# Performance work log

Measured on AMD Instinct MI355X. Metric: run time of the kernel, lower is better.

The kernel has to match this reference:

```python
import jax, jax.numpy as jnp
import numpy as np

N, E, H, C, F_IN, G = 20000, 320000, 8, 32, 41, 64
NEG_SLOPE = 0.2
BN_EPS = 1e-5


def setup_inputs() -> dict:
    key = jax.random.key(0)
    ks = jax.random.split(key, 32)
    s = 0.05
    d = {
        'x': jax.random.normal(ks[0], (N, F_IN), jnp.float32),
        'edge_index': jax.random.randint(ks[1], (2, E), 0, N, jnp.int32),
        'batch': jnp.sort(jax.random.randint(ks[2], (N,), 0, G, jnp.int32)),
        'graph_size': jax.random.uniform(ks[3], (G, 2), jnp.float32) * 10.0,
        'W1': jax.random.normal(ks[4], (F_IN, H * C), jnp.float32) * s,
        'a_src1': jax.random.normal(ks[5], (H, C), jnp.float32) * s,
        'a_dst1': jax.random.normal(ks[6], (H, C), jnp.float32) * s,
        'b1': jnp.zeros((H * C,), jnp.float32),
        'g1': jnp.ones((H * C,), jnp.float32),
        'be1': jnp.zeros((H * C,), jnp.float32),
        'W2': jax.random.normal(ks[7], (H * C, H * C), jnp.float32) * s,
        'a_src2': jax.random.normal(ks[8], (H, C), jnp.float32) * s,
        'a_dst2': jax.random.normal(ks[9], (H, C), jnp.float32) * s,
        'b2': jnp.zeros((H * C,), jnp.float32),
        'g2': jnp.ones((H * C,), jnp.float32),
        'be2': jnp.zeros((H * C,), jnp.float32),
        'fc1_w': jax.random.normal(ks[10], (2 * H * C + 2, 64), jnp.float32) * s,
        'fc1_b': jnp.zeros((64,), jnp.float32),
        'gf1': jnp.ones((64,), jnp.float32),
        'bf1': jnp.zeros((64,), jnp.float32),
        'fc2_w': jax.random.normal(ks[11], (64, 32), jnp.float32) * s,
        'fc2_b': jnp.zeros((32,), jnp.float32),
        'gf2': jnp.ones((32,), jnp.float32),
        'bf2': jnp.zeros((32,), jnp.float32),
        'fc3_w': jax.random.normal(ks[12], (32, 2), jnp.float32) * s,
        'fc3_b': jnp.zeros((2,), jnp.float32),
    }
    return d


def _bn_eval(x, gamma, beta):
    # eval-mode BatchNorm with running_mean=0, running_var=1
    inv = 1.0 / jnp.sqrt(1.0 + BN_EPS)
    return x * (gamma * inv) + beta


def _gat_layer(x, W, a_src, a_dst, bias, src, dst):
    h = (x @ W).reshape(N, H, C)                       # [N,H,C]
    s_src = jnp.einsum('nhc,hc->nh', h, a_src)         # [N,H]
    s_dst = jnp.einsum('nhc,hc->nh', h, a_dst)
    scores = jax.nn.leaky_relu(s_src[src] + s_dst[dst], NEG_SLOPE)  # [E+N,H]
    m = jax.ops.segment_max(scores, dst, num_segments=N)
    e = jnp.exp(scores - m[dst])
    denom = jax.ops.segment_sum(e, dst, num_segments=N)
    alpha = e / denom[dst]                             # [E+N,H]
    out = jax.ops.segment_sum(alpha[:, :, None] * h[src], dst, num_segments=N)
    return out.reshape(N, H * C) + bias


def reference(x, edge_index, batch, graph_size, W1, a_src1, a_dst1, b1, g1, be1,
              W2, a_src2, a_dst2, b2, g2, be2, fc1_w, fc1_b, gf1, bf1,
              fc2_w, fc2_b, gf2, bf2, fc3_w, fc3_b):
    # add self loops (PyG GATConv add_self_loops=True)
    loops = jnp.arange(N, dtype=edge_index.dtype)
    src = jnp.concatenate([edge_index[0], loops])
    dst = jnp.concatenate([edge_index[1], loops])

    h = _gat_layer(x, W1, a_src1, a_dst1, b1, src, dst)
    h = jax.nn.elu(_bn_eval(h, g1, be1))
    h = _gat_layer(h, W2, a_src2, a_dst2, b2, src, dst)
    h = jax.nn.elu(_bn_eval(h, g2, be2))

    # global mean + max pooling per graph
    counts = jax.ops.segment_sum(jnp.ones((N, 1), h.dtype), batch, num_segments=G)
    x_mean = jax.ops.segment_sum(h, batch, num_segments=G) / jnp.maximum(counts, 1.0)
    x_max = jax.ops.segment_max(h, batch, num_segments=G)
    p = jnp.concatenate([x_mean, x_max, graph_size], axis=1)  # [G, 514]

    z = jax.nn.relu(_bn_eval(p @ fc1_w + fc1_b, gf1, bf1))
    z = jax.nn.relu(_bn_eval(z @ fc2_w + fc2_b, gf2, bf2))
    logits = z @ fc3_w + fc3_b
    return logits
```

## Files before the change

kernel.cpp:

```cpp
#include <hip/hip_runtime.h>
#include <hip/hip_bf16.h>

#define N_NODES 20000
#define E_EDGES 320000
#define NH 8
#define NC 32
#define HC 256
#define FIN 41
#define NG 64
#define PCHUNK 16
#define NPAD 20032

typedef _Float16 f16x4 __attribute__((ext_vector_type(4)));
typedef _Float16 f16x8 __attribute__((ext_vector_type(8)));
typedef float f32x4v __attribute__((ext_vector_type(4)));


__global__ __launch_bounds__(512) void scanA(const int* __restrict__ cnt, int* partial) {
    __shared__ int red[512];
    int n = blockIdx.x * 512 + threadIdx.x;
    int v = (n < N_NODES) ? cnt[n] + 1 : 0;
    red[threadIdx.x] = v; __syncthreads();
    for (int off = 256; off > 0; off >>= 1) {
        if (threadIdx.x < off) red[threadIdx.x] += red[threadIdx.x + off];
        __syncthreads();
    }
    if (threadIdx.x == 0) partial[blockIdx.x] = red[0];
}

__global__ __launch_bounds__(512) void scanC(const int* __restrict__ cnt, const int* __restrict__ partial,
                                             int* row_ptr, int* cursor, int* colidx) {
    __shared__ int buf[512];
    __shared__ int pbase;
    int t = threadIdx.x;
    if (t < 64) {
        int v = (t < 40) ? partial[t] : 0;
        int own = v;
        for (int off = 1; off < 64; off <<= 1) {
            int y = __shfl_up(v, off);
            if (t >= off) v += y;
        }
        if (t == (int)blockIdx.x) pbase = v - own;
    }
    int n = blockIdx.x * 512 + t;
    int v = (n < N_NODES) ? cnt[n] + 1 : 0;
    int x = v;
    buf[t] = x; __syncthreads();
    for (int off = 1; off < 512; off <<= 1) {
        int y = (t >= off) ? buf[t - off] : 0;
        __syncthreads();
        x += y; buf[t] = x; __syncthreads();
    }
    int excl = pbase + x - v;
    if (n < N_NODES) {
        row_ptr[n] = excl;
        cursor[n] = excl + 1;
        colidx[excl] = n;
    }
    if (n == 0) row_ptr[N_NODES] = E_EDGES + N_NODES;
}

__global__ __launch_bounds__(256) void fill_csr(const int* __restrict__ ei, int* cursor, int* colidx) {
    int e = blockIdx.x * 256 + threadIdx.x;
    if (e >= E_EDGES) return;
    int d = ei[E_EDGES + e];
    int s = ei[e];
    int pos = atomicAdd(&cursor[d], 1);
    colidx[pos] = s;
}


__global__ __launch_bounds__(256) void prep(const float* __restrict__ W, _Float16* __restrict__ Wt,
                                            const float* __restrict__ fc1w, float* __restrict__ fc1wT,
                                            const int* __restrict__ batch, int* gstart, int* gend,
                                            const float* __restrict__ W1, _Float16* __restrict__ W1t,
                                            const float* __restrict__ x, _Float16* __restrict__ xpad,
                                            const int* __restrict__ ei, int* cnt) {
    __shared__ float tile[64][65];
    int b = blockIdx.x;
    int t = threadIdx.x;
    if (b < 16) {
        int tr = (b >> 2) * 64;
        int tc = (b & 3) * 64;
        int rr = t >> 6, cc = t & 63;
#pragma unroll
        for (int j = 0; j < 16; ++j) {
            int row = j * 4 + rr;
            tile[row][cc] = W[(size_t)(tr + row) * 256 + tc + cc];
        }
        __syncthreads();
#pragma unroll
        for (int j = 0; j < 16; ++j) {
            int row = j * 4 + rr;
            Wt[(size_t)(tc + row) * 256 + tr + cc] = (_Float16)tile[cc][row];
        }
    } else if (b < 145) {
        int id = (b - 16) * 256 + t;
        if (id < 64 * 514) {
            int u = id / 514, kk = id - u * 514;
            fc1wT[u * 520 + kk] = fc1w[kk * 64 + u];
        }
    } else if (b < 224) {
        int n = (b - 145) * 256 + t;
        if (n < N_NODES) {
            int bb = batch[n];
            if (n == 0) gstart[bb] = 0;
            else {
                int pb = batch[n - 1];
                if (pb != bb) { gstart[bb] = n; gend[pb] = n; }
            }
            if (n == N_NODES - 1) gend[bb] = N_NODES;
        }
    } else if (b < 288) {
        int id = (b - 224) * 256 + t;
        int n = id >> 6, k = id & 63;
        W1t[id] = (k < FIN) ? (_Float16)W1[k * 256 + n] : (_Float16)0.f;
    } else if (b < 914) {
        int row = (b - 288) * 32 + (t >> 3);
        int c8 = (t & 7) * 8;
        f16x8 v;
#pragma unroll
        for (int j = 0; j < 8; ++j) {
            int c = c8 + j;
            float f = (row < N_NODES && c < FIN) ? x[(size_t)row * FIN + c] : 0.f;
            v[j] = (_Float16)f;
        }
        if (row < NPAD) *(f16x8*)(xpad + (size_t)row * 64 + c8) = v;
    } else {
        int e = (b - 914) * 256 + t;
        if (e < E_EDGES) atomicAdd(&cnt[ei[E_EDGES + e]], 1);
    }
}


__global__ __launch_bounds__(256) void gemm256h(const _Float16* __restrict__ Xh,
                                                const _Float16* __restrict__ Wt,
                                                const float* __restrict__ a_src,
                                                const float* __restrict__ a_dst,
                                                _Float16* __restrict__ Hh,
                                                float* __restrict__ ssrc,
                                                float* __restrict__ sdst) {
    __shared__ _Float16 bs[128 * 272];
    int row0 = (blockIdx.x >> 1) * 64;
    int half = blockIdx.x & 1;
    int c0 = half * 128;
    int tid = threadIdx.x;
    int lane = tid & 63;
    int v = tid >> 6;
    int r16 = lane & 15;
    int kseg = lane >> 4;

#pragma unroll
    for (int i = 0; i < 16; ++i) {
        int chunk = i * 256 + tid;
        int c = chunk >> 5;
        int k = (chunk & 31) * 8;
        f16x8 xv = *(const f16x8*)(Wt + (size_t)(c0 + c) * 256 + k);
        *(f16x8*)(&bs[c * 272 + k]) = xv;
    }

    int arow = row0 + v * 16 + r16;
    const _Float16* XA = Xh + (size_t)arow * 256 + kseg * 8;
    f16x8 af[8];
#pragma unroll
    for (int s = 0; s < 8; ++s) af[s] = *(const f16x8*)(XA + s * 32);

    __syncthreads();

    f32x4v acc[8];
#pragma unroll
    for (int tn = 0; tn < 8; ++tn) acc[tn] = (f32x4v){0.f, 0.f, 0.f, 0.f};

#pragma unroll
    for (int tn = 0; tn < 8; ++tn) {
        f16x8 bf[8];
#pragma unroll
        for (int s = 0; s < 8; ++s)
            bf[s] = *(const f16x8*)(&bs[(tn * 16 + r16) * 272 + kseg * 8 + s * 32]);
#pragma unroll
        for (int s = 0; s < 8; ++s)
            acc[tn] = __builtin_amdgcn_mfma_f32_16x16x32_f16(af[s], bf[s], acc[tn], 0, 0, 0);
    }

#pragma unroll
    for (int hh = 0; hh < 4; ++hh) {
        float as0 = a_src[c0 + hh * 32 + r16], as1 = a_src[c0 + hh * 32 + 16 + r16];
        float ad0 = a_dst[c0 + hh * 32 + r16], ad1 = a_dst[c0 + hh * 32 + 16 + r16];
#pragma unroll
        for (int r = 0; r < 4; ++r) {
            float p = acc[2 * hh][r] * as0 + acc[2 * hh + 1][r] * as1;
            float q = acc[2 * hh][r] * ad0 + acc[2 * hh + 1][r] * ad1;
            p += __shfl_xor(p, 1); q += __shfl_xor(q, 1);
            p += __shfl_xor(p, 2); q += __shfl_xor(q, 2);
            p += __shfl_xor(p, 4); q += __shfl_xor(q, 4);
            p += __shfl_xor(p, 8); q += __shfl_xor(q, 8);
            int row = row0 + v * 16 + kseg * 4 + r;
            if (r16 == 0 && row < N_NODES) {
                ssrc[row * NH + half * 4 + hh] = p;
                sdst[row * NH + half * 4 + hh] = q;
            }
        }
    }

    __syncthreads();
    _Float16* hs = bs;
#pragma unroll
    for (int tn = 0; tn < 8; ++tn)
#pragma unroll
        for (int r = 0; r < 4; ++r)
            hs[(v * 16 + kseg * 4 + r) * 136 + tn * 16 + r16] = (_Float16)acc[tn][r];
    __syncthreads();
#pragma unroll
    for (int i = 0; i < 4; ++i) {
        int idx = i * 256 + tid;
        int row = idx >> 4;
        int c8 = (idx & 15) * 8;
        if (row0 + row < N_NODES) {
            f16x8 xv = *(const f16x8*)&hs[row * 136 + c8];
            *(f16x8*)(Hh + (size_t)(row0 + row) * 256 + c0 + c8) = xv;
        }
    }
}


__global__ __launch_bounds__(256) void gemm41h(const _Float16* __restrict__ Xh,
                                               const _Float16* __restrict__ W1t,
                                               const float* __restrict__ a_src,
                                               const float* __restrict__ a_dst,
                                               _Float16* __restrict__ Hh,
                                               float* __restrict__ ssrc,
                                               float* __restrict__ sdst) {
    __shared__ _Float16 bs[128 * 72];
    __shared__ _Float16 hs[64 * 136];
    int row0 = (blockIdx.x >> 1) * 64;
    int half = blockIdx.x & 1;
    int c0 = half * 128;
    int tid = threadIdx.x;
    int lane = tid & 63;
    int v = tid >> 6;
    int r16 = lane & 15;
    int kseg = lane >> 4;

#pragma unroll
    for (int i = 0; i < 4; ++i) {
        int chunk = i * 256 + tid;
        int c = chunk >> 3;
        int k = (chunk & 7) * 8;
        f16x8 xv = *(const f16x8*)(W1t + (size_t)(c0 + c) * 64 + k);
        *(f16x8*)(&bs[c * 72 + k]) = xv;
    }

    int arow = row0 + v * 16 + r16;
    const _Float16* XA = Xh + (size_t)arow * 64 + kseg * 8;
    f16x8 af[2];
    af[0] = *(const f16x8*)(XA);
    af[1] = *(const f16x8*)(XA + 32);

    __syncthreads();

    f32x4v acc[8];
#pragma unroll
    for (int tn = 0; tn < 8; ++tn) acc[tn] = (f32x4v){0.f, 0.f, 0.f, 0.f};

#pragma unroll
    for (int tn = 0; tn < 8; ++tn) {
        f16x8 bf0 = *(const f16x8*)(&bs[(tn * 16 + r16) * 72 + kseg * 8]);
        f16x8 bf1 = *(const f16x8*)(&bs[(tn * 16 + r16) * 72 + kseg * 8 + 32]);
        acc[tn] = __builtin_amdgcn_mfma_f32_16x16x32_f16(af[0], bf0, acc[tn], 0, 0, 0);
        acc[tn] = __builtin_amdgcn_mfma_f32_16x16x32_f16(af[1], bf1, acc[tn], 0, 0, 0);
    }

#pragma unroll
    for (int hh = 0; hh < 4; ++hh) {
        float as0 = a_src[c0 + hh * 32 + r16], as1 = a_src[c0 + hh * 32 + 16 + r16];
        float ad0 = a_dst[c0 + hh * 32 + r16], ad1 = a_dst[c0 + hh * 32 + 16 + r16];
#pragma unroll
        for (int r = 0; r < 4; ++r) {
            float p = acc[2 * hh][r] * as0 + acc[2 * hh + 1][r] * as1;
            float q = acc[2 * hh][r] * ad0 + acc[2 * hh + 1][r] * ad1;
            p += __shfl_xor(p, 1); q += __shfl_xor(q, 1);
            p += __shfl_xor(p, 2); q += __shfl_xor(q, 2);
            p += __shfl_xor(p, 4); q += __shfl_xor(q, 4);
            p += __shfl_xor(p, 8); q += __shfl_xor(q, 8);
            int row = row0 + v * 16 + kseg * 4 + r;
            if (r16 == 0 && row < N_NODES) {
                ssrc[row * NH + half * 4 + hh] = p;
                sdst[row * NH + half * 4 + hh] = q;
            }
        }
    }

    __syncthreads();
#pragma unroll
    for (int tn = 0; tn < 8; ++tn)
#pragma unroll
        for (int r = 0; r < 4; ++r)
            hs[(v * 16 + kseg * 4 + r) * 136 + tn * 16 + r16] = (_Float16)acc[tn][r];
    __syncthreads();
#pragma unroll
    for (int i = 0; i < 4; ++i) {
        int idx = i * 256 + tid;
        int row = idx >> 4;
        int c8 = (idx & 15) * 8;
        if (row0 + row < N_NODES) {
            f16x8 xv = *(const f16x8*)&hs[row * 136 + c8];
            *(f16x8*)(Hh + (size_t)(row0 + row) * 256 + c0 + c8) = xv;
        }
    }
}


__global__ __launch_bounds__(256) void gat_agg(const int* __restrict__ row_ptr,
                                               const int* __restrict__ colidx,
                                               const float* __restrict__ ssrc,
                                               const float* __restrict__ sdst,
                                               const _Float16* __restrict__ h,
                                               const float* __restrict__ bias,
                                               const float* __restrict__ gamma,
                                               const float* __restrict__ beta,
                                               _Float16* __restrict__ outh) {
    int wave = (blockIdx.x * blockDim.x + threadIdx.x) >> 6;
    int lane = threadIdx.x & 63;
    if (wave >= N_NODES) return;
    int n = wave;
    int beg = row_ptr[n], end = row_ptr[n + 1];
    int deg = end - beg;

    int hd = lane >> 3;
    float sd = sdst[n * NH + hd];
    int c = lane * 4;
    float acc0 = 0.f, acc1 = 0.f, acc2 = 0.f, acc3 = 0.f, denom = 0.f;

    int i = 0;
    for (; i + 8 <= deg; i += 8) {
        int sidx[8];
#pragma unroll
        for (int j = 0; j < 8; ++j) sidx[j] = colidx[beg + i + j];
        float wv[8];
#pragma unroll
        for (int j = 0; j < 8; ++j) {
            float v = ssrc[sidx[j] * NH + hd] + sd;
            v = (v >= 0.f) ? v : 0.2f * v;
            wv[j] = __expf(v);
        }
        f16x4 hv[8];
#pragma unroll
        for (int j = 0; j < 8; ++j) hv[j] = *reinterpret_cast<const f16x4*>(h + (size_t)sidx[j] * HC + c);
#pragma unroll
        for (int j = 0; j < 8; ++j) {
            denom += wv[j];
            acc0 += wv[j] * (float)hv[j][0];
            acc1 += wv[j] * (float)hv[j][1];
            acc2 += wv[j] * (float)hv[j][2];
            acc3 += wv[j] * (float)hv[j][3];
        }
    }
    for (; i < deg; ++i) {
        int s = colidx[beg + i];
        float v = ssrc[s * NH + hd] + sd;
        v = (v >= 0.f) ? v : 0.2f * v;
        float wgt = __expf(v);
        denom += wgt;
        const f16x4 hv = *reinterpret_cast<const f16x4*>(h + (size_t)s * HC + c);
        acc0 += wgt * (float)hv[0]; acc1 += wgt * (float)hv[1];
        acc2 += wgt * (float)hv[2]; acc3 += wgt * (float)hv[3];
    }
    float inv = 1.0f / denom;
    const float bninv = 0.99999500003749981f;
    float vals[4] = {acc0, acc1, acc2, acc3};
    f16x4 o;
#pragma unroll
    for (int j = 0; j < 4; ++j) {
        float v = vals[j] * inv + bias[c + j];
        v = v * (gamma[c + j] * bninv) + beta[c + j];
        v = (v > 0.f) ? v : (__expf(v) - 1.0f);
        o[j] = (_Float16)v;
    }
    *(f16x4*)(outh + (size_t)n * HC + c) = o;
}


__global__ __launch_bounds__(256) void pool_partial(const _Float16* __restrict__ h,
                                                    const int* __restrict__ gstart,
                                                    const int* __restrict__ gend,
                                                    float* __restrict__ psum,
                                                    float* __restrict__ pmax) {
    __shared__ float ssm[4][256];
    __shared__ float smx[4][256];
    int g = blockIdx.x >> 4;
    int c = blockIdx.x & (PCHUNK - 1);
    int t = threadIdx.x;
    int wv = t >> 6;
    int lane = t & 63;
    int c4 = lane * 4;
    int s = gstart[g], e = gend[g];
    int len = e - s;
    int n0 = s + (int)(((long long)len * c) / PCHUNK);
    int n1 = s + (int)(((long long)len * (c + 1)) / PCHUNK);
    float s0 = 0.f, s1 = 0.f, s2 = 0.f, s3 = 0.f;
    float m0 = -3.0e38f, m1 = -3.0e38f, m2 = -3.0e38f, m3 = -3.0e38f;
    for (int n = n0 + wv; n < n1; n += 4) {
        f16x4 v = *(const f16x4*)(h + (size_t)n * HC + c4);
        float f0 = (float)v[0], f1 = (float)v[1], f2 = (float)v[2], f3 = (float)v[3];
        s0 += f0; s1 += f1; s2 += f2; s3 += f3;
        m0 = fmaxf(m0, f0); m1 = fmaxf(m1, f1); m2 = fmaxf(m2, f2); m3 = fmaxf(m3, f3);
    }
    ssm[wv][c4] = s0; ssm[wv][c4 + 1] = s1; ssm[wv][c4 + 2] = s2; ssm[wv][c4 + 3] = s3;
    smx[wv][c4] = m0; smx[wv][c4 + 1] = m1; smx[wv][c4 + 2] = m2; smx[wv][c4 + 3] = m3;
    __syncthreads();
    float fs = ssm[0][t] + ssm[1][t] + ssm[2][t] + ssm[3][t];
    float fm = fmaxf(fmaxf(smx[0][t], smx[1][t]), fmaxf(smx[2][t], smx[3][t]));
    size_t base = (size_t)(g * PCHUNK + c) * HC + t;
    psum[base] = fs;
    pmax[base] = fm;
}


__global__ __launch_bounds__(256) void mlp(const float* __restrict__ psum,
                                           const float* __restrict__ pmax,
                                           const int* __restrict__ gstart,
                                           const int* __restrict__ gend,
                                           const float* __restrict__ gsz,
                                           const float* __restrict__ fc1wT, const float* __restrict__ fc1b,
                                           const float* __restrict__ gf1, const float* __restrict__ bf1,
                                           const float* __restrict__ fc2w, const float* __restrict__ fc2b,
                                           const float* __restrict__ gf2, const float* __restrict__ bf2,
                                           const float* __restrict__ fc3w, const float* __restrict__ fc3b,
                                           float* __restrict__ out) {
    __shared__ __align__(16) float pr[514];
    __shared__ float z1[64];
    __shared__ float zz2[8][32];
    __shared__ float z2[32];
    int g = blockIdx.x;
    int t = threadIdx.x;
    const float bninv = 0.99999500003749981f;

    {
        float s = 0.f, m = -3.0e38f;
#pragma unroll
        for (int c = 0; c < PCHUNK; ++c) {
            s += psum[(size_t)(g * PCHUNK + c) * HC + t];
            m = fmaxf(m, pmax[(size_t)(g * PCHUNK + c) * HC + t]);
        }
        float cnt = (float)(gend[g] - gstart[g]);
        pr[t] = s / fmaxf(cnt, 1.f);
        pr[256 + t] = m;
        if (t < 2) pr[512 + t] = gsz[g * 2 + t];
    }
    __syncthreads();

    {
        int wv = t >> 6, lane = t & 63;
        float4 pa = *reinterpret_cast<const float4*>(&pr[lane * 8]);
        float4 pb = *reinterpret_cast<const float4*>(&pr[lane * 8 + 4]);
#pragma unroll 4
        for (int i = 0; i < 16; ++i) {
            int u = wv * 16 + i;
            const float* wrow = fc1wT + u * 520;
            float4 wa = *reinterpret_cast<const float4*>(wrow + lane * 8);
            float4 wb = *reinterpret_cast<const float4*>(wrow + lane * 8 + 4);
            float a = pa.x * wa.x + pa.y * wa.y + pa.z * wa.z + pa.w * wa.w
                    + pb.x * wb.x + pb.y * wb.y + pb.z * wb.z + pb.w * wb.w;
            if (lane == 0) a += pr[512] * wrow[512] + pr[513] * wrow[513];
            a += __shfl_xor(a, 1); a += __shfl_xor(a, 2); a += __shfl_xor(a, 4);
            a += __shfl_xor(a, 8); a += __shfl_xor(a, 16); a += __shfl_xor(a, 32);
            if (lane == 0) {
                a += fc1b[u];
                a = a * (gf1[u] * bninv) + bf1[u];
                z1[u] = fmaxf(a, 0.f);
            }
        }
    }
    __syncthreads();

    {
        int u = t & 31, sp = t >> 5;
        float b = 0.f;
#pragma unroll
        for (int k = sp * 8; k < sp * 8 + 8; ++k) b += z1[k] * fc2w[k * 32 + u];
        zz2[sp][u] = b;
    }
    __syncthreads();
    if (t < 32) {
        float b = 0.f;
#pragma unroll
        for (int sp = 0; sp < 8; ++sp) b += zz2[sp][t];
        b += fc2b[t];
        b = b * (gf2[t] * bninv) + bf2[t];
        z2[t] = fmaxf(b, 0.f);
    }
    __syncthreads();

    if (t < 2) {
        float c = 0.f;
#pragma unroll
        for (int k = 0; k < 32; ++k) c += z2[k] * fc3w[k * 2 + t];
        out[g * 2 + t] = c + fc3b[t];
    }
}


extern "C" void kernel_launch(void* const* d_in, const int* in_sizes, int n_in,
                              void* d_out, int out_size, void* d_ws, size_t ws_size,
                              hipStream_t stream) {
    const float* x    = (const float*)d_in[0];
    const int*   ei   = (const int*)d_in[1];
    const int*   batch= (const int*)d_in[2];
    const float* gsz  = (const float*)d_in[3];
    const float* W1   = (const float*)d_in[4];
    const float* as1  = (const float*)d_in[5];
    const float* ad1  = (const float*)d_in[6];
    const float* b1   = (const float*)d_in[7];
    const float* g1   = (const float*)d_in[8];
    const float* be1  = (const float*)d_in[9];
    const float* W2   = (const float*)d_in[10];
    const float* as2  = (const float*)d_in[11];
    const float* ad2  = (const float*)d_in[12];
    const float* b2   = (const float*)d_in[13];
    const float* g2   = (const float*)d_in[14];
    const float* be2  = (const float*)d_in[15];
    const float* fc1w = (const float*)d_in[16];
    const float* fc1b = (const float*)d_in[17];
    const float* gf1  = (const float*)d_in[18];
    const float* bf1  = (const float*)d_in[19];
    const float* fc2w = (const float*)d_in[20];
    const float* fc2b = (const float*)d_in[21];
    const float* gf2  = (const float*)d_in[22];
    const float* bf2  = (const float*)d_in[23];
    const float* fc3w = (const float*)d_in[24];
    const float* fc3b = (const float*)d_in[25];
    float* out = (float*)d_out;

    char* w = (char*)d_ws;
    _Float16* h_half   = (_Float16*)w; w += (size_t)N_NODES * HC * 2;
    _Float16* act_half = (_Float16*)w; w += (size_t)N_NODES * HC * 2;
    _Float16* act2_half= (_Float16*)w; w += (size_t)N_NODES * HC * 2;
    _Float16* Wt       = (_Float16*)w; w += (size_t)HC * HC * 2;
    _Float16* W1t      = (_Float16*)w; w += (size_t)HC * 64 * 2;
    _Float16* xpad     = (_Float16*)w; w += (size_t)NPAD * 64 * 2;
    float* fc1wT       = (float*)w;    w += (size_t)64 * 520 * 4;
    float* ssrc        = (float*)w;    w += (size_t)N_NODES * NH * 4;
    float* sdst        = (float*)w;    w += (size_t)N_NODES * NH * 4;
    int* row_ptr  = (int*)w;   w += (size_t)(N_NODES + 1) * 4;
    int* cursor   = (int*)w;   w += (size_t)N_NODES * 4;
    int* cnt      = (int*)w;   w += (size_t)N_NODES * 4;
    int* gstart   = (int*)w;   w += 64 * 4;
    int* gend     = (int*)w;   w += 64 * 4;
    int* colidx   = (int*)w;   w += (size_t)(E_EDGES + N_NODES) * 4;
    int* partial  = (int*)w;   w += 64 * 4;

    float* psum = (float*)h_half;
    float* pmax = psum + (size_t)NG * PCHUNK * HC;

    hipMemsetAsync(cnt, 0, (size_t)(N_NODES + 128) * 4, stream);

    prep<<<2164, 256, 0, stream>>>(W2, Wt, fc1w, fc1wT, batch, gstart, gend, W1, W1t, x, xpad, ei, cnt);
    scanA<<<40, 512, 0, stream>>>(cnt, partial);
    scanC<<<40, 512, 0, stream>>>(cnt, partial, row_ptr, cursor, colidx);
    fill_csr<<<1250, 256, 0, stream>>>(ei, cursor, colidx);

    gemm41h<<<626, 256, 0, stream>>>(xpad, W1t, as1, ad1, h_half, ssrc, sdst);
    gat_agg<<<5000, 256, 0, stream>>>(row_ptr, colidx, ssrc, sdst, h_half, b1, g1, be1, act_half);

    gemm256h<<<626, 256, 0, stream>>>(act_half, Wt, as2, ad2, h_half, ssrc, sdst);
    gat_agg<<<5000, 256, 0, stream>>>(row_ptr, colidx, ssrc, sdst, h_half, b2, g2, be2, act2_half);

    pool_partial<<<NG * PCHUNK, 256, 0, stream>>>(act2_half, gstart, gend, psum, pmax);
    mlp<<<NG, 256, 0, stream>>>(psum, pmax, gstart, gend, gsz,
                                fc1wT, fc1b, gf1, bf1, fc2w, fc2b, gf2, bf2, fc3w, fc3b, out);
}
```

Before: 160.6 us.

## Fuse CSR fill into first GEMM launch and store attention scores in fp16

Merges the CSR fill kernel into the layer-1 GEMM launch as extra blocks, so the edge scatter runs alongside the GEMM and one launch is removed. Separately, the per-node source/destination attention scores are stored as fp16 instead of fp32, halving the bytes for the random gathers in the aggregation kernels. The fp16 scores lose some precision before leaky-relu and exp, which could shift softmax weights slightly.

```diff
diff --git a/kernel.cpp b/kernel.cpp
--- a/kernel.cpp
+++ b/kernel.cpp
@@ -58,15 +58,6 @@
         colidx[excl] = n;
     }
     if (n == 0) row_ptr[N_NODES] = E_EDGES + N_NODES;
-}
-
-__global__ __launch_bounds__(256) void fill_csr(const int* __restrict__ ei, int* cursor, int* colidx) {
-    int e = blockIdx.x * 256 + threadIdx.x;
-    if (e >= E_EDGES) return;
-    int d = ei[E_EDGES + e];
-    int s = ei[e];
-    int pos = atomicAdd(&cursor[d], 1);
-    colidx[pos] = s;
 }
 
 
@@ -138,8 +129,8 @@
                                                 const float* __restrict__ a_src,
                                                 const float* __restrict__ a_dst,
                                                 _Float16* __restrict__ Hh,
-                                                float* __restrict__ ssrc,
-                                                float* __restrict__ sdst) {
+                                                _Float16* __restrict__ ssrc,
+                                                _Float16* __restrict__ sdst) {
     __shared__ _Float16 bs[128 * 272];
     int row0 = (blockIdx.x >> 1) * 64;
     int half = blockIdx.x & 1;
@@ -196,8 +187,8 @@
             p += __shfl_xor(p, 8); q += __shfl_xor(q, 8);
             int row = row0 + v * 16 + kseg * 4 + r;
             if (r16 == 0 && row < N_NODES) {
-                ssrc[row * NH + half * 4 + hh] = p;
-                sdst[row * NH + half * 4 + hh] = q;
+                ssrc[row * NH + half * 4 + hh] = (_Float16)p;
+                sdst[row * NH + half * 4 + hh] = (_Float16)q;
             }
         }
     }
@@ -223,19 +214,34 @@
 }
 
 
-__global__ __launch_bounds__(256) void gemm41h(const _Float16* __restrict__ Xh,
-                                               const _Float16* __restrict__ W1t,
-                                               const float* __restrict__ a_src,
-                                               const float* __restrict__ a_dst,
-                                               _Float16* __restrict__ Hh,
-                                               float* __restrict__ ssrc,
-                                               float* __restrict__ sdst) {
+__global__ __launch_bounds__(256) void gemm41_fill(const _Float16* __restrict__ Xh,
+                                                   const _Float16* __restrict__ W1t,
+                                                   const float* __restrict__ a_src,
+                                                   const float* __restrict__ a_dst,
+                                                   _Float16* __restrict__ Hh,
+                                                   _Float16* __restrict__ ssrc,
+                                                   _Float16* __restrict__ sdst,
+                                                   const int* __restrict__ ei,
+                                                   int* cursor, int* colidx) {
     __shared__ _Float16 bs[128 * 72];
     __shared__ _Float16 hs[64 * 136];
-    int row0 = (blockIdx.x >> 1) * 64;
-    int half = blockIdx.x & 1;
+    int b = blockIdx.x;
+    int tid = threadIdx.x;
+
+    if (b >= 626) {
+        int e = (b - 626) * 256 + tid;
+        if (e < E_EDGES) {
+            int d = ei[E_EDGES + e];
+            int s = ei[e];
+            int pos = atomicAdd(&cursor[d], 1);
+            colidx[pos] = s;
+        }
+        return;
+    }
+
+    int row0 = (b >> 1) * 64;
+    int half = b & 1;
     int c0 = half * 128;
-    int tid = threadIdx.x;
     int lane = tid & 63;
     int v = tid >> 6;
     int r16 = lane & 15;
@@ -284,8 +290,8 @@
             p += __shfl_xor(p, 8); q += __shfl_xor(q, 8);
             int row = row0 + v * 16 + kseg * 4 + r;
             if (r16 == 0 && row < N_NODES) {
-                ssrc[row * NH + half * 4 + hh] = p;
-                sdst[row * NH + half * 4 + hh] = q;
+                ssrc[row * NH + half * 4 + hh] = (_Float16)p;
+                sdst[row * NH + half * 4 + hh] = (_Float16)q;
             }
         }
     }
@@ -312,8 +318,8 @@
 
 __global__ __launch_bounds__(256) void gat_agg(const int* __restrict__ row_ptr,
                                                const int* __restrict__ colidx,
-                                               const float* __restrict__ ssrc,
-                                               const float* __restrict__ sdst,
+                                               const _Float16* __restrict__ ssrc,
+                                               const _Float16* __restrict__ sdst,
                                                const _Float16* __restrict__ h,
                                                const float* __restrict__ bias,
                                                const float* __restrict__ gamma,
@@ -327,7 +333,7 @@
     int deg = end - beg;
 
     int hd = lane >> 3;
-    float sd = sdst[n * NH + hd];
+    float sd = (float)sdst[n * NH + hd];
     int c = lane * 4;
     float acc0 = 0.f, acc1 = 0.f, acc2 = 0.f, acc3 = 0.f, denom = 0.f;
 
@@ -339,7 +345,7 @@
         float wv[8];
 #pragma unroll
         for (int j = 0; j < 8; ++j) {
-            float v = ssrc[sidx[j] * NH + hd] + sd;
+            float v = (float)ssrc[sidx[j] * NH + hd] + sd;
             v = (v >= 0.f) ? v : 0.2f * v;
             wv[j] = __expf(v);
         }
@@ -357,7 +363,7 @@
     }
     for (; i < deg; ++i) {
         int s = colidx[beg + i];
-        float v = ssrc[s * NH + hd] + sd;
+        float v = (float)ssrc[s * NH + hd] + sd;
         v = (v >= 0.f) ? v : 0.2f * v;
         float wgt = __expf(v);
         denom += wgt;
@@ -539,8 +545,8 @@
     _Float16* W1t      = (_Float16*)w; w += (size_t)HC * 64 * 2;
     _Float16* xpad     = (_Float16*)w; w += (size_t)NPAD * 64 * 2;
     float* fc1wT       = (float*)w;    w += (size_t)64 * 520 * 4;
-    float* ssrc        = (float*)w;    w += (size_t)N_NODES * NH * 4;
-    float* sdst        = (float*)w;    w += (size_t)N_NODES * NH * 4;
+    _Float16* ssrc     = (_Float16*)w; w += (size_t)N_NODES * NH * 2;
+    _Float16* sdst     = (_Float16*)w; w += (size_t)N_NODES * NH * 2;
     int* row_ptr  = (int*)w;   w += (size_t)(N_NODES + 1) * 4;
     int* cursor   = (int*)w;   w += (size_t)N_NODES * 4;
     int* cnt      = (int*)w;   w += (size_t)N_NODES * 4;
@@ -557,9 +563,8 @@
     prep<<<2164, 256, 0, stream>>>(W2, Wt, fc1w, fc1wT, batch, gstart, gend, W1, W1t, x, xpad, ei, cnt);
     scanA<<<40, 512, 0, stream>>>(cnt, partial);
     scanC<<<40, 512, 0, stream>>>(cnt, partial, row_ptr, cursor, colidx);
-    fill_csr<<<1250, 256, 0, stream>>>(ei, cursor, colidx);
-
-    gemm41h<<<626, 256, 0, stream>>>(xpad, W1t, as1, ad1, h_half, ssrc, sdst);
+
+    gemm41_fill<<<1876, 256, 0, stream>>>(xpad, W1t, as1, ad1, h_half, ssrc, sdst, ei, cursor, colidx);
     gat_agg<<<5000, 256, 0, stream>>>(row_ptr, colidx, ssrc, sdst, h_half, b1, g1, be1, act_half);
 
     gemm256h<<<626, 256, 0, stream>>>(act_half, Wt, as2, ad2, h_half, ssrc, sdst);
```

After: 151.1 us. 5.9% less time.
